# Performance work log

Hardware: AMD Instinct MI355X
Metric: run time of the kernel (lower is better)

## Reference

```python
import jax, jax.numpy as jnp
import numpy as np
from jax import lax

N_LINKS = 10000
N_PATHS = 100000
PATH_LEN = 8   # max_seq_len (all paths padded to this)
H = 32         # link/path state dim and GRU hidden size
RD = 8         # readout dim
T = 8          # message-passing rounds


def setup_inputs() -> dict:
    key = jax.random.key(0)
    ks = jax.random.split(key, 20)
    E = N_PATHS * PATH_LEN
    links = jax.random.randint(ks[0], (E,), 0, N_LINKS)
    paths = jnp.repeat(jnp.arange(N_PATHS), PATH_LEN)
    seqs = jnp.tile(jnp.arange(PATH_LEN), N_PATHS)
    link_capacity = jax.random.uniform(ks[1], (N_LINKS,), dtype=jnp.float32)
    bandwith = jax.random.uniform(ks[2], (N_PATHS,), dtype=jnp.float32)
    s = 1.0 / np.sqrt(H)
    u = lambda k, shp: jax.random.uniform(k, shp, minval=-s, maxval=s, dtype=jnp.float32)
    return {
        'links': links, 'paths': paths, 'seqs': seqs,
        'link_capacity': link_capacity, 'bandwith': bandwith,
        # path GRU (p_U) params, torch layout: [3H, in] with gate order r,z,n
        'p_Wih': u(ks[3], (3 * H, H)), 'p_Whh': u(ks[4], (3 * H, H)),
        'p_bih': u(ks[5], (3 * H,)), 'p_bhh': u(ks[6], (3 * H,)),
        # link GRU (l_U) params
        'l_Wih': u(ks[7], (3 * H, H)), 'l_Whh': u(ks[8], (3 * H, H)),
        'l_bih': u(ks[9], (3 * H,)), 'l_bhh': u(ks[10], (3 * H,)),
        # readout MLP
        'W1': u(ks[11], (RD, H)), 'b1': u(ks[12], (RD,)),
        'W2': u(ks[13], (RD, RD)), 'b2': u(ks[14], (RD,)),
        'W3': u(ks[15], (1, RD)), 'b3': u(ks[16], (1,)),
    }


def gru_cell(x, h, Wih, Whh, bih, bhh):
    # torch GRU cell: gates in order (reset, update, new)
    gi = x @ Wih.T + bih   # [N, 3H]
    gh = h @ Whh.T + bhh   # [N, 3H]
    i_r, i_z, i_n = jnp.split(gi, 3, axis=-1)
    h_r, h_z, h_n = jnp.split(gh, 3, axis=-1)
    r = jax.nn.sigmoid(i_r + h_r)
    z = jax.nn.sigmoid(i_z + h_z)
    n = jnp.tanh(i_n + r * h_n)
    return (1.0 - z) * n + z * h


def reference(links, paths, seqs, link_capacity, bandwith,
              p_Wih, p_Whh, p_bih, p_bhh,
              l_Wih, l_Whh, l_bih, l_bhh,
              W1, b1, W2, b2, W3, b3):
    dt = link_capacity.dtype
    # initial states: feature 0 is capacity / bandwidth, rest zeros
    link_state = jnp.concatenate(
        [link_capacity[:, None], jnp.zeros((N_LINKS, H - 1), dt)], axis=1)
    path_state = jnp.concatenate(
        [bandwith[:, None], jnp.zeros((N_PATHS, H - 1), dt)], axis=1)

    def path_step(h, x_t):
        h2 = gru_cell(x_t, h, p_Wih, p_Whh, p_bih, p_bhh)
        return h2, h2

    for _ in range(T):
        # gather link states onto path hops: [E, H]
        gathered = link_state[links]
        # scatter into dense padded path-RNN input [n_paths, L, H]
        rnn_in = jnp.zeros((N_PATHS, PATH_LEN, H), dt).at[paths, seqs].set(gathered)
        # path GRU over the padded sequence, initial hidden = path_state
        path_state, hs = lax.scan(path_step, path_state,
                                  jnp.swapaxes(rnn_in, 0, 1))  # hs: [L, n_paths, H]
        # per-hop messages back to links, then scatter-add per link
        link_msgs = hs[seqs, paths]                            # [E, H]
        agg = jax.ops.segment_sum(link_msgs, links, num_segments=N_LINKS)
        # link GRU single step: input = aggregated message, hidden = link_state
        link_state = gru_cell(agg, link_state, l_Wih, l_Whh, l_bih, l_bhh)

    # readout MLP on final path state
    x = jax.nn.relu(path_state @ W1.T + b1)
    x = jax.nn.relu(x @ W2.T + b2)
    return x @ W3.T + b3  # [n_paths, 1]
```

## Files before the change

### kernel.cpp

```cpp
#include <hip/hip_runtime.h>
#include <hip/hip_bf16.h>

#define NL 10000
#define NP 100000
#define PLEN 8
#define H 32
#define NROUNDS 8
#define E_TOT (NP * PLEN)

typedef float f2 __attribute__((ext_vector_type(2)));
typedef float f4 __attribute__((ext_vector_type(4)));
typedef short bh8 __attribute__((ext_vector_type(8)));

#define LINK_OFF   0
#define PATH_OFF   320000
#define AGG_OFF    3520000
#define WTS_OFF    3840000
#define PW_OFF     3853400
#define FLAG_OFF   3869000
#define INT_OFF    3870000
#define HS_OFF     4700032
#define WS_NEED_FLOATS (HS_OFF + (size_t)E_TOT * H)

#define LOG2E 1.44269504f


__device__ __forceinline__ float bf2f(unsigned short u) {
  union { unsigned int i; float f; } v; v.i = ((unsigned int)u) << 16; return v.f;
}
__device__ __forceinline__ float fast_exp2(float x) {
#if __has_builtin(__builtin_amdgcn_exp2f)
  return __builtin_amdgcn_exp2f(x);
#else
  return __expf(x * 0.69314718f);
#endif
}
__device__ __forceinline__ float fast_rcp(float x) {
#if __has_builtin(__builtin_amdgcn_rcpf)
  return __builtin_amdgcn_rcpf(x);
#else
  return 1.f / x;
#endif
}
__device__ __forceinline__ float fast_sigm(float x) {
  return fast_rcp(1.f + fast_exp2(-LOG2E * x));
}
__device__ __forceinline__ float fast_tanh2(float x) {
  return 1.f - 2.f * fast_rcp(1.f + fast_exp2((2.f * LOG2E) * x));
}
__device__ __forceinline__ float loadf(const void* p, long i, bool bf) {
  return bf ? bf2f(((const unsigned short*)p)[i]) : ((const float*)p)[i];
}

__device__ __forceinline__ void split8(f4 a, f4 b, bh8& hi, bh8& lo) {
  #pragma unroll
  for (int i = 0; i < 4; ++i) {
    unsigned ua = __float_as_uint(a[i]);
    float hfa = __uint_as_float(ua & 0xffff0000u);
    hi[i] = (short)(ua >> 16);
    lo[i] = (short)(__float_as_uint(a[i] - hfa) >> 16);
    unsigned ub = __float_as_uint(b[i]);
    float hfb = __uint_as_float(ub & 0xffff0000u);
    hi[4 + i] = (short)(ub >> 16);
    lo[4 + i] = (short)(__float_as_uint(b[i] - hfb) >> 16);
  }
}

__global__ void probe_dtype(const unsigned int* __restrict__ cap_words,
                            int* __restrict__ flag) {
  int lane = threadIdx.x;
  int c = 0;
  #pragma unroll
  for (int i = 0; i < 4; ++i) {
    unsigned int b = (cap_words[lane * 4 + i] >> 8) & 0xFF;
    if (b >= 0x30 && b < 0x40) ++c;
  }
  #pragma unroll
  for (int d = 32; d > 0; d >>= 1) c += __shfl_down(c, d);
  if (lane == 0) *flag = (c > 128) ? 1 : 0;
}

__device__ __forceinline__ void gru_cell_f2(const float* __restrict__ W,
                                            const f2 x[16], f2 h[16]) {
  const f2* Wih = (const f2*)W;
  const f2* Whh = (const f2*)(W + 3072);
  const float* bih = W + 6144;
  const float* bhh = W + 6240;
  f2 hn[16];
  #pragma unroll
  for (int jj = 0; jj < 16; ++jj) {
    #pragma unroll
    for (int s = 0; s < 2; ++s) {
      const int j = 2 * jj + s;
      f2 ar = {0.f, 0.f}, az = {0.f, 0.f}, an = {0.f, 0.f}, ah = {0.f, 0.f};
      #pragma unroll
      for (int k = 0; k < 16; ++k) {
        ar = __builtin_elementwise_fma(Wih[j * 16 + k], x[k], ar);
        ar = __builtin_elementwise_fma(Whh[j * 16 + k], h[k], ar);
        az = __builtin_elementwise_fma(Wih[(H + j) * 16 + k], x[k], az);
        az = __builtin_elementwise_fma(Whh[(H + j) * 16 + k], h[k], az);
        an = __builtin_elementwise_fma(Wih[(2 * H + j) * 16 + k], x[k], an);
        ah = __builtin_elementwise_fma(Whh[(2 * H + j) * 16 + k], h[k], ah);
      }
      float r = fast_sigm(ar.x + ar.y + bih[j] + bhh[j]);
      float z = fast_sigm(az.x + az.y + bih[H + j] + bhh[H + j]);
      float n = fast_tanh2(an.x + an.y + bih[2 * H + j] +
                           r * (ah.x + ah.y + bhh[2 * H + j]));
      float hold = (s == 0) ? h[jj].x : h[jj].y;
      float hv = n + z * (hold - n);
      if (s == 0) hn[jj].x = hv; else hn[jj].y = hv;
    }
  }
  #pragma unroll
  for (int k = 0; k < 16; ++k) h[k] = hn[k];
}

struct BfSeg { const void* src; int dstoff; int len; };
struct BfSegs { BfSeg s[14]; };
struct WPack { unsigned short* p[8]; };

__global__ void convert_weights(BfSegs segs, WPack wp, const int* __restrict__ flag,
                                float* __restrict__ dst) {
  const bool bf = (*flag != 0);
  const int si = blockIdx.x;
  const void* p = segs.s[si].src;
  const int off = segs.s[si].dstoff, len = segs.s[si].len;
  int hix = -1;
  if (si == 0) hix = 0; else if (si == 1) hix = 2;
  else if (si == 4) hix = 4; else if (si == 5) hix = 6;
  for (int i = threadIdx.x; i < len; i += blockDim.x) {
    float f = loadf(p, i, bf);
    dst[off + i] = f;
    if (hix >= 0) {
      unsigned u = __float_as_uint(f);
      float fh = __uint_as_float(u & 0xffff0000u);
      wp.p[hix][i] = (unsigned short)(u >> 16);
      wp.p[hix + 1][i] = (unsigned short)(__float_as_uint(f - fh) >> 16);
    }
  }
}

__global__ void init_states(const void* __restrict__ cap,
                            const void* __restrict__ bw,
                            const int* __restrict__ flag,
                            float* __restrict__ link_state,
                            unsigned short* __restrict__ lhi,
                            unsigned short* __restrict__ llo,
                            float* __restrict__ path_state) {
  const bool bf = (*flag != 0);
  int i = blockIdx.x * blockDim.x + threadIdx.x;
  if (i < NP * H) path_state[i] = ((i & (H - 1)) == 0) ? loadf(bw, i >> 5, bf) : 0.f;
  if (i < NL * H) {
    float v = ((i & (H - 1)) == 0) ? loadf(cap, i >> 5, bf) : 0.f;
    link_state[i] = v;
    unsigned u = __float_as_uint(v);
    float fh = __uint_as_float(u & 0xffff0000u);
    lhi[i] = (unsigned short)(u >> 16);
    llo[i] = (unsigned short)(__float_as_uint(v - fh) >> 16);
  }
}

__global__ void csr_count(const int* __restrict__ links, int* __restrict__ counts) {
  int e = blockIdx.x * blockDim.x + threadIdx.x;
  if (e < E_TOT) atomicAdd(&counts[links[e]], 1);
}

__global__ __launch_bounds__(256) void csr_scan(const int* __restrict__ counts,
                                                int* __restrict__ offsets,
                                                int* __restrict__ cursor) {
  __shared__ int part[256];
  const int t = threadIdx.x;
  const int base = t * 40;
  int s = 0;
  for (int i = 0; i < 40; ++i) {
    int idx = base + i;
    if (idx < NL) s += counts[idx];
  }
  part[t] = s;
  __syncthreads();
  for (int d = 1; d < 256; d <<= 1) {
    int v = (t >= d) ? part[t - d] : 0;
    __syncthreads();
    part[t] += v;
    __syncthreads();
  }
  int run = (t > 0) ? part[t - 1] : 0;
  for (int i = 0; i < 40; ++i) {
    int idx = base + i;
    if (idx < NL) {
      offsets[idx] = run;
      cursor[idx] = run;
      run += counts[idx];
    }
  }
  if (t == 255) offsets[NL] = run;
}

__global__ void csr_fill(const int* __restrict__ links, int* __restrict__ cursor,
                         int* __restrict__ perm) {
  int e = blockIdx.x * blockDim.x + threadIdx.x;
  if (e < E_TOT) {
    int l = links[e];
    int pos = atomicAdd(&cursor[l], 1);
    perm[e] = pos;
  }
}

template <int LAST>
__global__ __launch_bounds__(256) void path_round_mfma(
    const int* __restrict__ links, const int* __restrict__ perm,
    const unsigned short* __restrict__ lhi, const unsigned short* __restrict__ llo,
    float* __restrict__ path_state, float* __restrict__ hs,
    const float* __restrict__ W,
    const unsigned short* __restrict__ wih_hi, const unsigned short* __restrict__ wih_lo,
    const unsigned short* __restrict__ whh_hi, const unsigned short* __restrict__ whh_lo,
    const int* __restrict__ flag, void* __restrict__ out) {
  __shared__ float lds_all[4 * 16 * 36];
  const int wv = threadIdx.x >> 6;
  const int tile = blockIdx.x * 4 + wv;
  if (tile >= NP / 16) return;
  const int p0 = tile * 16;
  const int lane = threadIdx.x & 63;
  const int c = lane & 15, q = lane >> 4, m = c;
  float* lds = lds_all + wv * (16 * 36);

  bh8 wihH[6], wihL[6], whhH[6], whhL[6];
  #pragma unroll
  for (int tn = 0; tn < 6; ++tn) {
    size_t o = (size_t)(tn * 16 + c) * H + q * 8;
    wihH[tn] = *(const bh8*)(wih_hi + o);
    wihL[tn] = *(const bh8*)(wih_lo + o);
    whhH[tn] = *(const bh8*)(whh_hi + o);
    whhL[tn] = *(const bh8*)(whh_lo + o);
  }
  const float* bih = W + 6144;
  const float* bhh = W + 6240;
  float b_r[2], b_z[2], b_in[2], b_hn[2];
  #pragma unroll
  for (int u2 = 0; u2 < 2; ++u2) {
    int u = u2 * 16 + c;
    b_r[u2] = bih[u] + bhh[u];
    b_z[u2] = bih[32 + u] + bhh[32 + u];
    b_in[u2] = bih[64 + u];
    b_hn[u2] = bhh[64 + u];
  }
  float hC[2][4];
  #pragma unroll
  for (int u2 = 0; u2 < 2; ++u2)
    #pragma unroll
    for (int rg = 0; rg < 4; ++rg)
      hC[u2][rg] = path_state[(size_t)(p0 + q * 4 + rg) * H + u2 * 16 + c];
  f4 hfa = *(const f4*)(path_state + (size_t)(p0 + m) * H + q * 8);
  f4 hfb = *(const f4*)(path_state + (size_t)(p0 + m) * H + q * 8 + 4);
  bh8 hhi, hlo;
  split8(hfa, hfb, hhi, hlo);
  int lk[PLEN], pm[PLEN];
  {
    const int4* lp = (const int4*)(links + (size_t)(p0 + m) * PLEN);
    int4 a = lp[0], b = lp[1];
    lk[0] = a.x; lk[1] = a.y; lk[2] = a.z; lk[3] = a.w;
    lk[4] = b.x; lk[5] = b.y; lk[6] = b.z; lk[7] = b.w;
    if (!LAST) {
      const int4* qp = (const int4*)(perm + (size_t)(p0 + m) * PLEN);
      int4 e = qp[0], f = qp[1];
      pm[0] = e.x; pm[1] = e.y; pm[2] = e.z; pm[3] = e.w;
      pm[4] = f.x; pm[5] = f.y; pm[6] = f.z; pm[7] = f.w;
    }
  }
  bh8 xhi = *(const bh8*)(lhi + (size_t)lk[0] * H + q * 8);
  bh8 xlo = *(const bh8*)(llo + (size_t)lk[0] * H + q * 8);
  const f4 z4 = {0.f, 0.f, 0.f, 0.f};

  #pragma unroll 1
  for (int t = 0; t < PLEN; ++t) {
    bh8 xnhi, xnlo;
    if (t + 1 < PLEN) {
      xnhi = *(const bh8*)(lhi + (size_t)lk[t + 1] * H + q * 8);
      xnlo = *(const bh8*)(llo + (size_t)lk[t + 1] * H + q * 8);
    }
    f4 aR[2], aZ[2], aI[2], aHn[2];
    #pragma unroll
    for (int u2 = 0; u2 < 2; ++u2) {
      f4 a = z4;
      a = __builtin_amdgcn_mfma_f32_16x16x32_bf16(xhi, wihH[u2], a, 0, 0, 0);
      a = __builtin_amdgcn_mfma_f32_16x16x32_bf16(hhi, whhH[u2], a, 0, 0, 0);
      a = __builtin_amdgcn_mfma_f32_16x16x32_bf16(xlo, wihH[u2], a, 0, 0, 0);
      a = __builtin_amdgcn_mfma_f32_16x16x32_bf16(hlo, whhH[u2], a, 0, 0, 0);
      a = __builtin_amdgcn_mfma_f32_16x16x32_bf16(xhi, wihL[u2], a, 0, 0, 0);
      a = __builtin_amdgcn_mfma_f32_16x16x32_bf16(hhi, whhL[u2], a, 0, 0, 0);
      aR[u2] = a;
      f4 b = z4;
      b = __builtin_amdgcn_mfma_f32_16x16x32_bf16(xhi, wihH[2 + u2], b, 0, 0, 0);
      b = __builtin_amdgcn_mfma_f32_16x16x32_bf16(hhi, whhH[2 + u2], b, 0, 0, 0);
      b = __builtin_amdgcn_mfma_f32_16x16x32_bf16(xlo, wihH[2 + u2], b, 0, 0, 0);
      b = __builtin_amdgcn_mfma_f32_16x16x32_bf16(hlo, whhH[2 + u2], b, 0, 0, 0);
      b = __builtin_amdgcn_mfma_f32_16x16x32_bf16(xhi, wihL[2 + u2], b, 0, 0, 0);
      b = __builtin_amdgcn_mfma_f32_16x16x32_bf16(hhi, whhL[2 + u2], b, 0, 0, 0);
      aZ[u2] = b;
      f4 ci = z4;
      ci = __builtin_amdgcn_mfma_f32_16x16x32_bf16(xhi, wihH[4 + u2], ci, 0, 0, 0);
      ci = __builtin_amdgcn_mfma_f32_16x16x32_bf16(xlo, wihH[4 + u2], ci, 0, 0, 0);
      ci = __builtin_amdgcn_mfma_f32_16x16x32_bf16(xhi, wihL[4 + u2], ci, 0, 0, 0);
      aI[u2] = ci;
      f4 ch = z4;
      ch = __builtin_amdgcn_mfma_f32_16x16x32_bf16(hhi, whhH[4 + u2], ch, 0, 0, 0);
      ch = __builtin_amdgcn_mfma_f32_16x16x32_bf16(hlo, whhH[4 + u2], ch, 0, 0, 0);
      ch = __builtin_amdgcn_mfma_f32_16x16x32_bf16(hhi, whhL[4 + u2], ch, 0, 0, 0);
      aHn[u2] = ch;
    }
    #pragma unroll
    for (int u2 = 0; u2 < 2; ++u2)
      #pragma unroll
      for (int rg = 0; rg < 4; ++rg) {
        float rr = fast_sigm(aR[u2][rg] + b_r[u2]);
        float zz = fast_sigm(aZ[u2][rg] + b_z[u2]);
        float nn = fast_tanh2(fmaf(rr, aHn[u2][rg] + b_hn[u2], aI[u2][rg] + b_in[u2]));
        float hv = fmaf(zz, hC[u2][rg] - nn, nn);
        hC[u2][rg] = hv;
        lds[(q * 4 + rg) * 36 + u2 * 16 + c] = hv;
      }
    __builtin_amdgcn_wave_barrier();
    __builtin_amdgcn_s_waitcnt(0xC07F);
    f4 ha = *(const f4*)(lds + m * 36 + q * 8);
    f4 hb = *(const f4*)(lds + m * 36 + q * 8 + 4);
    __builtin_amdgcn_wave_barrier();
    if (!LAST) {
      float* hp = hs + (size_t)pm[t] * H + q * 8;
      *(f4*)hp = ha;
      *(f4*)(hp + 4) = hb;
    }
    if (t + 1 < PLEN) {
      split8(ha, hb, hhi, hlo);
      xhi = xnhi; xlo = xnlo;
    } else if (LAST) {
      const float* RW = W + 12672;
      float part[8];
      #pragma unroll
      for (int i = 0; i < 8; ++i) {
        const f4* w4 = (const f4*)(RW + i * 32 + q * 8);
        f4 wa = w4[0], wb = w4[1];
        part[i] = wa[0] * ha[0] + wa[1] * ha[1] + wa[2] * ha[2] + wa[3] * ha[3]
                + wb[0] * hb[0] + wb[1] * hb[1] + wb[2] * hb[2] + wb[3] * hb[3];
      }
      #pragma unroll
      for (int i = 0; i < 8; ++i) {
        part[i] += __shfl_xor(part[i], 16);
        part[i] += __shfl_xor(part[i], 32);
      }
      if (q == 0) {
        float y1[8], y2[8];
        #pragma unroll
        for (int i = 0; i < 8; ++i) y1[i] = fmaxf(part[i] + RW[256 + i], 0.f);
        #pragma unroll
        for (int i = 0; i < 8; ++i) {
          float a = RW[328 + i];
          #pragma unroll
          for (int k = 0; k < 8; ++k) a = fmaf(RW[264 + i * 8 + k], y1[k], a);
          y2[i] = fmaxf(a, 0.f);
        }
        float o = RW[344];
        #pragma unroll
        for (int k = 0; k < 8; ++k) o = fmaf(RW[336 + k], y2[k], o);
        if (*flag) ((__hip_bfloat16*)out)[p0 + m] = __float2bfloat16(o);
        else       ((float*)out)[p0 + m] = o;
      }
    } else {
      float* pp = path_state + (size_t)(p0 + m) * H + q * 8;
      *(f4*)pp = ha;
      *(f4*)(pp + 4) = hb;
    }
  }
}

__global__ __launch_bounds__(256) void agg_link_round(
    const int* __restrict__ offsets,
    const float* __restrict__ hs, float* __restrict__ link_state,
    unsigned short* __restrict__ lhi, unsigned short* __restrict__ llo,
    const float* __restrict__ W,
    const unsigned short* __restrict__ wih_hi, const unsigned short* __restrict__ wih_lo,
    const unsigned short* __restrict__ whh_hi, const unsigned short* __restrict__ whh_lo) {
  __shared__ float aggL[16 * 36];
  const int l0 = blockIdx.x * 16;
  const int wv = threadIdx.x >> 6;
  const int lane = threadIdx.x & 63;
  #pragma unroll 1
  for (int s = 0; s < 4; ++s) {
    const int li = wv * 4 + s;
    const int l = l0 + li;
    const int beg = offsets[l], end = offsets[l + 1];
    const f4* base4 = (const f4*)(hs + (size_t)beg * H);
    const int nvec = (end - beg) * (H / 4);
    f4 a0 = {0.f, 0.f, 0.f, 0.f}, a1 = {0.f, 0.f, 0.f, 0.f};
    int i = lane;
    for (; i + 64 < nvec; i += 128) {
      a0 += base4[i];
      a1 += base4[i + 64];
    }
    if (i < nvec) a0 += base4[i];
    a0 += a1;
    #pragma unroll
    for (int d = 32; d >= 8; d >>= 1) {
      #pragma unroll
      for (int k = 0; k < 4; ++k) a0[k] += __shfl_xor(a0[k], d);
    }
    if (lane < 8) *(f4*)(aggL + li * 36 + 4 * lane) = a0;
  }
  __syncthreads();
  if (threadIdx.x >= 64) return;
  const int c = lane & 15, q = lane >> 4, m = c;
  bh8 wihH[6], wihL[6], whhH[6], whhL[6];
  #pragma unroll
  for (int tn = 0; tn < 6; ++tn) {
    size_t o = (size_t)(tn * 16 + c) * H + q * 8;
    wihH[tn] = *(const bh8*)(wih_hi + o);
    wihL[tn] = *(const bh8*)(wih_lo + o);
    whhH[tn] = *(const bh8*)(whh_hi + o);
    whhL[tn] = *(const bh8*)(whh_lo + o);
  }
  const float* bih = W + 6144;
  const float* bhh = W + 6240;
  float b_r[2], b_z[2], b_in[2], b_hn[2];
  #pragma unroll
  for (int u2 = 0; u2 < 2; ++u2) {
    int u = u2 * 16 + c;
    b_r[u2] = bih[u] + bhh[u];
    b_z[u2] = bih[32 + u] + bhh[32 + u];
    b_in[u2] = bih[64 + u];
    b_hn[u2] = bhh[64 + u];
  }
  float hC[2][4];
  #pragma unroll
  for (int u2 = 0; u2 < 2; ++u2)
    #pragma unroll
    for (int rg = 0; rg < 4; ++rg)
      hC[u2][rg] = link_state[(size_t)(l0 + q * 4 + rg) * H + u2 * 16 + c];
  f4 xa = *(const f4*)(aggL + m * 36 + q * 8);
  f4 xb = *(const f4*)(aggL + m * 36 + q * 8 + 4);
  f4 hfa = *(const f4*)(link_state + (size_t)(l0 + m) * H + q * 8);
  f4 hfb = *(const f4*)(link_state + (size_t)(l0 + m) * H + q * 8 + 4);
  bh8 xhi, xlo, hhi, hlo;
  split8(xa, xb, xhi, xlo);
  split8(hfa, hfb, hhi, hlo);
  const f4 z4 = {0.f, 0.f, 0.f, 0.f};
  f4 aR[2], aZ[2], aI[2], aHn[2];
  #pragma unroll
  for (int u2 = 0; u2 < 2; ++u2) {
    f4 a = z4;
    a = __builtin_amdgcn_mfma_f32_16x16x32_bf16(xhi, wihH[u2], a, 0, 0, 0);
    a = __builtin_amdgcn_mfma_f32_16x16x32_bf16(hhi, whhH[u2], a, 0, 0, 0);
    a = __builtin_amdgcn_mfma_f32_16x16x32_bf16(xlo, wihH[u2], a, 0, 0, 0);
    a = __builtin_amdgcn_mfma_f32_16x16x32_bf16(hlo, whhH[u2], a, 0, 0, 0);
    a = __builtin_amdgcn_mfma_f32_16x16x32_bf16(xhi, wihL[u2], a, 0, 0, 0);
    a = __builtin_amdgcn_mfma_f32_16x16x32_bf16(hhi, whhL[u2], a, 0, 0, 0);
    aR[u2] = a;
    f4 b = z4;
    b = __builtin_amdgcn_mfma_f32_16x16x32_bf16(xhi, wihH[2 + u2], b, 0, 0, 0);
    b = __builtin_amdgcn_mfma_f32_16x16x32_bf16(hhi, whhH[2 + u2], b, 0, 0, 0);
    b = __builtin_amdgcn_mfma_f32_16x16x32_bf16(xlo, wihH[2 + u2], b, 0, 0, 0);
    b = __builtin_amdgcn_mfma_f32_16x16x32_bf16(hlo, whhH[2 + u2], b, 0, 0, 0);
    b = __builtin_amdgcn_mfma_f32_16x16x32_bf16(xhi, wihL[2 + u2], b, 0, 0, 0);
    b = __builtin_amdgcn_mfma_f32_16x16x32_bf16(hhi, whhL[2 + u2], b, 0, 0, 0);
    aZ[u2] = b;
    f4 ci = z4;
    ci = __builtin_amdgcn_mfma_f32_16x16x32_bf16(xhi, wihH[4 + u2], ci, 0, 0, 0);
    ci = __builtin_amdgcn_mfma_f32_16x16x32_bf16(xlo, wihH[4 + u2], ci, 0, 0, 0);
    ci = __builtin_amdgcn_mfma_f32_16x16x32_bf16(xhi, wihL[4 + u2], ci, 0, 0, 0);
    aI[u2] = ci;
    f4 ch = z4;
    ch = __builtin_amdgcn_mfma_f32_16x16x32_bf16(hhi, whhH[4 + u2], ch, 0, 0, 0);
    ch = __builtin_amdgcn_mfma_f32_16x16x32_bf16(hlo, whhH[4 + u2], ch, 0, 0, 0);
    ch = __builtin_amdgcn_mfma_f32_16x16x32_bf16(hhi, whhL[4 + u2], ch, 0, 0, 0);
    aHn[u2] = ch;
  }
  #pragma unroll
  for (int u2 = 0; u2 < 2; ++u2)
    #pragma unroll
    for (int rg = 0; rg < 4; ++rg) {
      float rr = fast_sigm(aR[u2][rg] + b_r[u2]);
      float zz = fast_sigm(aZ[u2][rg] + b_z[u2]);
      float nn = fast_tanh2(fmaf(rr, aHn[u2][rg] + b_hn[u2], aI[u2][rg] + b_in[u2]));
      float hv = fmaf(zz, hC[u2][rg] - nn, nn);
      size_t idx = (size_t)(l0 + q * 4 + rg) * H + u2 * 16 + c;
      link_state[idx] = hv;
      unsigned u = __float_as_uint(hv);
      float fh = __uint_as_float(u & 0xffff0000u);
      lhi[idx] = (unsigned short)(u >> 16);
      llo[idx] = (unsigned short)(__float_as_uint(hv - fh) >> 16);
    }
}

__global__ __launch_bounds__(64) void path_round_atomic(
    const int* __restrict__ links, const float* __restrict__ link_state,
    float* __restrict__ path_state, float* __restrict__ agg,
    const float* __restrict__ W, int do_scatter) {
  int p = blockIdx.x * 64 + threadIdx.x;
  if (p >= NP) return;
  f2 h[16];
  const f2* ps2 = (const f2*)(path_state + (size_t)p * H);
  #pragma unroll
  for (int k = 0; k < 16; ++k) h[k] = ps2[k];
  int lk[PLEN];
  const int4* lp = (const int4*)(links + (size_t)p * PLEN);
  int4 la = lp[0], lb = lp[1];
  lk[0] = la.x; lk[1] = la.y; lk[2] = la.z; lk[3] = la.w;
  lk[4] = lb.x; lk[5] = lb.y; lk[6] = lb.z; lk[7] = lb.w;
  #pragma unroll 1
  for (int t = 0; t < PLEN; ++t) {
    const f2* xs = (const f2*)(link_state + (size_t)lk[t] * H);
    f2 x[16];
    #pragma unroll
    for (int k = 0; k < 16; ++k) x[k] = xs[k];
    gru_cell_f2(W, x, h);
    if (do_scatter) {
      float* dst = agg + (size_t)lk[t] * H;
      #pragma unroll
      for (int k = 0; k < 16; ++k) {
        unsafeAtomicAdd(dst + 2 * k, h[k].x);
        unsafeAtomicAdd(dst + 2 * k + 1, h[k].y);
      }
    }
  }
  f2* po = (f2*)(path_state + (size_t)p * H);
  #pragma unroll
  for (int k = 0; k < 16; ++k) po[k] = h[k];
}

__global__ __launch_bounds__(64) void link_round_scalar(
    const float* __restrict__ agg, float* __restrict__ link_state,
    const float* __restrict__ W) {
  int li = blockIdx.x * 64 + threadIdx.x;
  if (li >= NL) return;
  f2 x[16], h[16];
  const f2* xa = (const f2*)(agg + (size_t)li * H);
  f2* hsrow = (f2*)(link_state + (size_t)li * H);
  #pragma unroll
  for (int k = 0; k < 16; ++k) { x[k] = xa[k]; h[k] = hsrow[k]; }
  gru_cell_f2(W, x, h);
  #pragma unroll
  for (int k = 0; k < 16; ++k) hsrow[k] = h[k];
}

__global__ __launch_bounds__(256) void readout_kernel(
    const float* __restrict__ path_state, const float* __restrict__ W,
    const int* __restrict__ flag, void* __restrict__ out) {
  int p = blockIdx.x * 256 + threadIdx.x;
  if (p >= NP) return;
  const float* W1 = W;
  const float* b1 = W + 256;
  const float* W2 = W + 264;
  const float* b2 = W + 328;
  const float* W3 = W + 336;
  const float* b3 = W + 344;
  float xv[32];
  const float4* xp = (const float4*)(path_state + (size_t)p * H);
  #pragma unroll
  for (int k = 0; k < 8; ++k) {
    float4 v = xp[k];
    xv[4 * k] = v.x; xv[4 * k + 1] = v.y; xv[4 * k + 2] = v.z; xv[4 * k + 3] = v.w;
  }
  float y1[8];
  #pragma unroll
  for (int i = 0; i < 8; ++i) {
    float a = b1[i];
    #pragma unroll
    for (int k = 0; k < 32; ++k) a = fmaf(W1[i * 32 + k], xv[k], a);
    y1[i] = fmaxf(a, 0.f);
  }
  float y2[8];
  #pragma unroll
  for (int i = 0; i < 8; ++i) {
    float a = b2[i];
    #pragma unroll
    for (int k = 0; k < 8; ++k) a = fmaf(W2[i * 8 + k], y1[k], a);
    y2[i] = fmaxf(a, 0.f);
  }
  float o = b3[0];
  #pragma unroll
  for (int k = 0; k < 8; ++k) o = fmaf(W3[k], y2[k], o);
  if (*flag) ((__hip_bfloat16*)out)[p] = __float2bfloat16(o);
  else       ((float*)out)[p] = o;
}

extern "C" void kernel_launch(void* const* d_in, const int* in_sizes, int n_in,
                              void* d_out, int out_size, void* d_ws, size_t ws_size,
                              hipStream_t stream) {
  (void)in_sizes; (void)n_in; (void)out_size;
  const int* links = (const int*)d_in[0];
  const void* cap = d_in[3];
  const void* bw  = d_in[4];

  float* ws = (float*)d_ws;
  float* link_state = ws + LINK_OFF;
  float* path_state = ws + PATH_OFF;
  float* agg        = ws + AGG_OFF;
  unsigned short* lhi = (unsigned short*)(ws + AGG_OFF);
  unsigned short* llo = (unsigned short*)(ws + AGG_OFF + 160000);
  float* wts        = ws + WTS_OFF;
  int*   flag       = (int*)(ws + FLAG_OFF);
  int*   ibase      = (int*)(ws + INT_OFF);
  int*   counts     = ibase;
  int*   offsets    = ibase + 10000;
  int*   cursor     = ibase + 20016;
  int*   perm       = ibase + 30016;
  float* hs         = ws + HS_OFF;

  WPack wp;
  for (int i = 0; i < 8; ++i)
    wp.p[i] = (unsigned short*)(ws + PW_OFF + i * 1600);

  const bool use_gather = ws_size >= WS_NEED_FLOATS * sizeof(float);

  probe_dtype<<<1, 64, 0, stream>>>((const unsigned int*)cap, flag);

  BfSegs segs;
  const int srcidx[14] = {5, 6, 7, 8, 9, 10, 11, 12, 13, 14, 15, 16, 17, 18};
  const int offs[14]   = {0, 3072, 6144, 6240, 6336, 9408, 12480, 12576,
                          12672, 12928, 12936, 13000, 13008, 13016};
  const int lens[14]   = {3072, 3072, 96, 96, 3072, 3072, 96, 96,
                          256, 8, 64, 8, 8, 1};
  for (int i = 0; i < 14; ++i) {
    segs.s[i].src = d_in[srcidx[i]];
    segs.s[i].dstoff = offs[i];
    segs.s[i].len = lens[i];
  }
  convert_weights<<<14, 256, 0, stream>>>(segs, wp, flag, wts);
  init_states<<<(NP * H + 255) / 256, 256, 0, stream>>>(
      cap, bw, flag, link_state, lhi, llo, path_state);

  if (use_gather) {
    hipMemsetAsync(counts, 0, NL * sizeof(int), stream);
    csr_count<<<(E_TOT + 255) / 256, 256, 0, stream>>>(links, counts);
    csr_scan<<<1, 256, 0, stream>>>(counts, offsets, cursor);
    csr_fill<<<(E_TOT + 255) / 256, 256, 0, stream>>>(links, cursor, perm);

    const int path_blocks = (NP / 16 + 3) / 4;
    for (int r = 0; r < NROUNDS - 1; ++r) {
      path_round_mfma<0><<<path_blocks, 256, 0, stream>>>(
          links, perm, lhi, llo, path_state, hs, wts,
          wp.p[0], wp.p[1], wp.p[2], wp.p[3], flag, d_out);
      agg_link_round<<<NL / 16, 256, 0, stream>>>(
          offsets, hs, link_state, lhi, llo,
          wts + 6336, wp.p[4], wp.p[5], wp.p[6], wp.p[7]);
    }
    path_round_mfma<1><<<path_blocks, 256, 0, stream>>>(
        links, perm, lhi, llo, path_state, hs, wts,
        wp.p[0], wp.p[1], wp.p[2], wp.p[3], flag, d_out);
  } else {
    for (int r = 0; r < NROUNDS; ++r) {
      const int last = (r == NROUNDS - 1);
      if (!last) hipMemsetAsync(agg, 0, NL * H * sizeof(float), stream);
      path_round_atomic<<<(NP + 63) / 64, 64, 0, stream>>>(
          links, link_state, path_state, agg, wts, !last);
      if (!last)
        link_round_scalar<<<(NL + 63) / 64, 64, 0, stream>>>(agg, link_state, wts + 6336);
    }
    readout_kernel<<<(NP + 255) / 256, 256, 0, stream>>>(
        path_state, wts + 12672, flag, d_out);
  }
}
```

Baseline: 777.7 us.

## Process two 16-path tiles per wave in path GRU kernel for ILP

New measurement: 935.0 us. 20.2% more time.

```diff
diff --git a/kernel.cpp b/kernel.cpp
--- a/kernel.cpp
+++ b/kernel.cpp
@@ -215,14 +215,13 @@
     const unsigned short* __restrict__ wih_hi, const unsigned short* __restrict__ wih_lo,
     const unsigned short* __restrict__ whh_hi, const unsigned short* __restrict__ whh_lo,
     const int* __restrict__ flag, void* __restrict__ out) {
-  __shared__ float lds_all[4 * 16 * 36];
+  __shared__ float lds_all[4 * 2 * 16 * 36];
   const int wv = threadIdx.x >> 6;
-  const int tile = blockIdx.x * 4 + wv;
-  if (tile >= NP / 16) return;
-  const int p0 = tile * 16;
+  const int pair = blockIdx.x * 4 + wv;
+  if (pair >= NP / 32) return;
   const int lane = threadIdx.x & 63;
   const int c = lane & 15, q = lane >> 4, m = c;
-  float* lds = lds_all + wv * (16 * 36);
+  float* ldsw = lds_all + wv * (2 * 16 * 36);
 
   bh8 wihH[6], wihL[6], whhH[6], whhL[6];
   #pragma unroll
@@ -244,130 +243,157 @@
     b_in[u2] = bih[64 + u];
     b_hn[u2] = bhh[64 + u];
   }
-  float hC[2][4];
-  #pragma unroll
-  for (int u2 = 0; u2 < 2; ++u2)
-    #pragma unroll
-    for (int rg = 0; rg < 4; ++rg)
-      hC[u2][rg] = path_state[(size_t)(p0 + q * 4 + rg) * H + u2 * 16 + c];
-  f4 hfa = *(const f4*)(path_state + (size_t)(p0 + m) * H + q * 8);
-  f4 hfb = *(const f4*)(path_state + (size_t)(p0 + m) * H + q * 8 + 4);
-  bh8 hhi, hlo;
-  split8(hfa, hfb, hhi, hlo);
-  int lk[PLEN], pm[PLEN];
-  {
-    const int4* lp = (const int4*)(links + (size_t)(p0 + m) * PLEN);
-    int4 a = lp[0], b = lp[1];
-    lk[0] = a.x; lk[1] = a.y; lk[2] = a.z; lk[3] = a.w;
-    lk[4] = b.x; lk[5] = b.y; lk[6] = b.z; lk[7] = b.w;
-    if (!LAST) {
-      const int4* qp = (const int4*)(perm + (size_t)(p0 + m) * PLEN);
-      int4 e = qp[0], f = qp[1];
-      pm[0] = e.x; pm[1] = e.y; pm[2] = e.z; pm[3] = e.w;
-      pm[4] = f.x; pm[5] = f.y; pm[6] = f.z; pm[7] = f.w;
-    }
-  }
-  bh8 xhi = *(const bh8*)(lhi + (size_t)lk[0] * H + q * 8);
-  bh8 xlo = *(const bh8*)(llo + (size_t)lk[0] * H + q * 8);
+
+  const int prow0 = pair * 32;
+  int pbase[2] = {prow0 + m, prow0 + 16 + m};
+
+  float hC[2][2][4];
+  bh8 hhi[2], hlo[2], xhi[2], xlo[2];
+  int iA[2];
+  #pragma unroll
+  for (int tt = 0; tt < 2; ++tt) {
+    const int prow = prow0 + tt * 16;
+    #pragma unroll
+    for (int u2 = 0; u2 < 2; ++u2)
+      #pragma unroll
+      for (int rg = 0; rg < 4; ++rg)
+        hC[tt][u2][rg] = path_state[(size_t)(prow + q * 4 + rg) * H + u2 * 16 + c];
+    f4 hfa = *(const f4*)(path_state + (size_t)(prow + m) * H + q * 8);
+    f4 hfb = *(const f4*)(path_state + (size_t)(prow + m) * H + q * 8 + 4);
+    split8(hfa, hfb, hhi[tt], hlo[tt]);
+    int i0 = links[(size_t)pbase[tt] * PLEN + 0];
+    iA[tt]  = links[(size_t)pbase[tt] * PLEN + 1];
+    xhi[tt] = *(const bh8*)(lhi + (size_t)i0 * H + q * 8);
+    xlo[tt] = *(const bh8*)(llo + (size_t)i0 * H + q * 8);
+  }
   const f4 z4 = {0.f, 0.f, 0.f, 0.f};
 
   #pragma unroll 1
   for (int t = 0; t < PLEN; ++t) {
-    bh8 xnhi, xnlo;
-    if (t + 1 < PLEN) {
-      xnhi = *(const bh8*)(lhi + (size_t)lk[t + 1] * H + q * 8);
-      xnlo = *(const bh8*)(llo + (size_t)lk[t + 1] * H + q * 8);
-    }
-    f4 aR[2], aZ[2], aI[2], aHn[2];
-    #pragma unroll
-    for (int u2 = 0; u2 < 2; ++u2) {
-      f4 a = z4;
-      a = __builtin_amdgcn_mfma_f32_16x16x32_bf16(xhi, wihH[u2], a, 0, 0, 0);
-      a = __builtin_amdgcn_mfma_f32_16x16x32_bf16(hhi, whhH[u2], a, 0, 0, 0);
-      a = __builtin_amdgcn_mfma_f32_16x16x32_bf16(xlo, wihH[u2], a, 0, 0, 0);
-      a = __builtin_amdgcn_mfma_f32_16x16x32_bf16(hlo, whhH[u2], a, 0, 0, 0);
-      a = __builtin_amdgcn_mfma_f32_16x16x32_bf16(xhi, wihL[u2], a, 0, 0, 0);
-      a = __builtin_amdgcn_mfma_f32_16x16x32_bf16(hhi, whhL[u2], a, 0, 0, 0);
-      aR[u2] = a;
-      f4 b = z4;
-      b = __builtin_amdgcn_mfma_f32_16x16x32_bf16(xhi, wihH[2 + u2], b, 0, 0, 0);
-      b = __builtin_amdgcn_mfma_f32_16x16x32_bf16(hhi, whhH[2 + u2], b, 0, 0, 0);
-      b = __builtin_amdgcn_mfma_f32_16x16x32_bf16(xlo, wihH[2 + u2], b, 0, 0, 0);
-      b = __builtin_amdgcn_mfma_f32_16x16x32_bf16(hlo, whhH[2 + u2], b, 0, 0, 0);
-      b = __builtin_amdgcn_mfma_f32_16x16x32_bf16(xhi, wihL[2 + u2], b, 0, 0, 0);
-      b = __builtin_amdgcn_mfma_f32_16x16x32_bf16(hhi, whhL[2 + u2], b, 0, 0, 0);
-      aZ[u2] = b;
-      f4 ci = z4;
-      ci = __builtin_amdgcn_mfma_f32_16x16x32_bf16(xhi, wihH[4 + u2], ci, 0, 0, 0);
-      ci = __builtin_amdgcn_mfma_f32_16x16x32_bf16(xlo, wihH[4 + u2], ci, 0, 0, 0);
-      ci = __builtin_amdgcn_mfma_f32_16x16x32_bf16(xhi, wihL[4 + u2], ci, 0, 0, 0);
-      aI[u2] = ci;
-      f4 ch = z4;
-      ch = __builtin_amdgcn_mfma_f32_16x16x32_bf16(hhi, whhH[4 + u2], ch, 0, 0, 0);
-      ch = __builtin_amdgcn_mfma_f32_16x16x32_bf16(hlo, whhH[4 + u2], ch, 0, 0, 0);
-      ch = __builtin_amdgcn_mfma_f32_16x16x32_bf16(hhi, whhL[4 + u2], ch, 0, 0, 0);
-      aHn[u2] = ch;
-    }
-    #pragma unroll
-    for (int u2 = 0; u2 < 2; ++u2)
-      #pragma unroll
-      for (int rg = 0; rg < 4; ++rg) {
-        float rr = fast_sigm(aR[u2][rg] + b_r[u2]);
-        float zz = fast_sigm(aZ[u2][rg] + b_z[u2]);
-        float nn = fast_tanh2(fmaf(rr, aHn[u2][rg] + b_hn[u2], aI[u2][rg] + b_in[u2]));
-        float hv = fmaf(zz, hC[u2][rg] - nn, nn);
-        hC[u2][rg] = hv;
-        lds[(q * 4 + rg) * 36 + u2 * 16 + c] = hv;
-      }
+    int pmt[2], iB[2];
+    bh8 xnhi[2], xnlo[2];
+    #pragma unroll
+    for (int tt = 0; tt < 2; ++tt) {
+      if (!LAST) pmt[tt] = perm[(size_t)pbase[tt] * PLEN + t];
+      iB[tt] = (t + 2 < PLEN) ? links[(size_t)pbase[tt] * PLEN + t + 2] : iA[tt];
+      if (t + 1 < PLEN) {
+        xnhi[tt] = *(const bh8*)(lhi + (size_t)iA[tt] * H + q * 8);
+        xnlo[tt] = *(const bh8*)(llo + (size_t)iA[tt] * H + q * 8);
+      }
+    }
+    f4 aR[2][2], aZ[2][2], aI[2][2], aHn[2][2];
+    #pragma unroll
+    for (int tt = 0; tt < 2; ++tt)
+      #pragma unroll
+      for (int u2 = 0; u2 < 2; ++u2) {
+        f4 a = z4;
+        a = __builtin_amdgcn_mfma_f32_16x16x32_bf16(xhi[tt], wihH[u2], a, 0, 0, 0);
+        a = __builtin_amdgcn_mfma_f32_16x16x32_bf16(hhi[tt], whhH[u2], a, 0, 0, 0);
+        a = __builtin_amdgcn_mfma_f32_16x16x32_bf16(xlo[tt], wihH[u2], a, 0, 0, 0);
+        a = __builtin_amdgcn_mfma_f32_16x16x32_bf16(hlo[tt], whhH[u2], a, 0, 0, 0);
+        a = __builtin_amdgcn_mfma_f32_16x16x32_bf16(xhi[tt], wihL[u2], a, 0, 0, 0);
+        a = __builtin_amdgcn_mfma_f32_16x16x32_bf16(hhi[tt], whhL[u2], a, 0, 0, 0);
+        aR[tt][u2] = a;
+        f4 b = z4;
+        b = __builtin_amdgcn_mfma_f32_16x16x32_bf16(xhi[tt], wihH[2 + u2], b, 0, 0, 0);
+        b = __builtin_amdgcn_mfma_f32_16x16x32_bf16(hhi[tt], whhH[2 + u2], b, 0, 0, 0);
+        b = __builtin_amdgcn_mfma_f32_16x16x32_bf16(xlo[tt], wihH[2 + u2], b, 0, 0, 0);
+        b = __builtin_amdgcn_mfma_f32_16x16x32_bf16(hlo[tt], whhH[2 + u2], b, 0, 0, 0);
+        b = __builtin_amdgcn_mfma_f32_16x16x32_bf16(xhi[tt], wihL[2 + u2], b, 0, 0, 0);
+        b = __builtin_amdgcn_mfma_f32_16x16x32_bf16(hhi[tt], whhL[2 + u2], b, 0, 0, 0);
+        aZ[tt][u2] = b;
+        f4 ci = z4;
+        ci = __builtin_amdgcn_mfma_f32_16x16x32_bf16(xhi[tt], wihH[4 + u2], ci, 0, 0, 0);
+        ci = __builtin_amdgcn_mfma_f32_16x16x32_bf16(xlo[tt], wihH[4 + u2], ci, 0, 0, 0);
+        ci = __builtin_amdgcn_mfma_f32_16x16x32_bf16(xhi[tt], wihL[4 + u2], ci, 0, 0, 0);
+        aI[tt][u2] = ci;
+        f4 ch = z4;
+        ch = __builtin_amdgcn_mfma_f32_16x16x32_bf16(hhi[tt], whhH[4 + u2], ch, 0, 0, 0);
+        ch = __builtin_amdgcn_mfma_f32_16x16x32_bf16(hlo[tt], whhH[4 + u2], ch, 0, 0, 0);
+        ch = __builtin_amdgcn_mfma_f32_16x16x32_bf16(hhi[tt], whhL[4 + u2], ch, 0, 0, 0);
+        aHn[tt][u2] = ch;
+      }
+    #pragma unroll
+    for (int tt = 0; tt < 2; ++tt)
+      #pragma unroll
+      for (int u2 = 0; u2 < 2; ++u2)
+        #pragma unroll
+        for (int rg = 0; rg < 4; ++rg) {
+          float rr = fast_sigm(aR[tt][u2][rg] + b_r[u2]);
+          float zz = fast_sigm(aZ[tt][u2][rg] + b_z[u2]);
+          float nn = fast_tanh2(fmaf(rr, aHn[tt][u2][rg] + b_hn[u2],
+                                     aI[tt][u2][rg] + b_in[u2]));
+          float hv = fmaf(zz, hC[tt][u2][rg] - nn, nn);
+          hC[tt][u2][rg] = hv;
+          ldsw[tt * 576 + (q * 4 + rg) * 36 + u2 * 16 + c] = hv;
+        }
     __builtin_amdgcn_wave_barrier();
     __builtin_amdgcn_s_waitcnt(0xC07F);
-    f4 ha = *(const f4*)(lds + m * 36 + q * 8);
-    f4 hb = *(const f4*)(lds + m * 36 + q * 8 + 4);
+    f4 ha[2], hb[2];
+    #pragma unroll
+    for (int tt = 0; tt < 2; ++tt) {
+      ha[tt] = *(const f4*)(ldsw + tt * 576 + m * 36 + q * 8);
+      hb[tt] = *(const f4*)(ldsw + tt * 576 + m * 36 + q * 8 + 4);
+    }
     __builtin_amdgcn_wave_barrier();
     if (!LAST) {
-      float* hp = hs + (size_t)pm[t] * H + q * 8;
-      *(f4*)hp = ha;
-      *(f4*)(hp + 4) = hb;
+      #pragma unroll
+      for (int tt = 0; tt < 2; ++tt) {
+        float* hp = hs + (size_t)pmt[tt] * H + q * 8;
+        *(f4*)hp = ha[tt];
+        *(f4*)(hp + 4) = hb[tt];
+      }
     }
     if (t + 1 < PLEN) {
-      split8(ha, hb, hhi, hlo);
-      xhi = xnhi; xlo = xnlo;
+      #pragma unroll
+      for (int tt = 0; tt < 2; ++tt) {
+        split8(ha[tt], hb[tt], hhi[tt], hlo[tt]);
+        xhi[tt] = xnhi[tt]; xlo[tt] = xnlo[tt];
+        iA[tt] = iB[tt];
+      }
     } else if (LAST) {
       const float* RW = W + 12672;
-      float part[8];
-      #pragma unroll
-      for (int i = 0; i < 8; ++i) {
-        const f4* w4 = (const f4*)(RW + i * 32 + q * 8);
-        f4 wa = w4[0], wb = w4[1];
-        part[i] = wa[0] * ha[0] + wa[1] * ha[1] + wa[2] * ha[2] + wa[3] * ha[3]
-                + wb[0] * hb[0] + wb[1] * hb[1] + wb[2] * hb[2] + wb[3] * hb[3];
-      }
-      #pragma unroll
-      for (int i = 0; i < 8; ++i) {
-        part[i] += __shfl_xor(part[i], 16);
-        part[i] += __shfl_xor(part[i], 32);
-      }
-      if (q == 0) {
-        float y1[8], y2[8];
-        #pragma unroll
-        for (int i = 0; i < 8; ++i) y1[i] = fmaxf(part[i] + RW[256 + i], 0.f);
+      #pragma unroll
+      for (int tt = 0; tt < 2; ++tt) {
+        float part[8];
         #pragma unroll
         for (int i = 0; i < 8; ++i) {
-          float a = RW[328 + i];
+          const f4* w4 = (const f4*)(RW + i * 32 + q * 8);
+          f4 wa = w4[0], wb = w4[1];
+          part[i] = wa[0] * ha[tt][0] + wa[1] * ha[tt][1] + wa[2] * ha[tt][2] +
+                    wa[3] * ha[tt][3] + wb[0] * hb[tt][0] + wb[1] * hb[tt][1] +
+                    wb[2] * hb[tt][2] + wb[3] * hb[tt][3];
+        }
+        #pragma unroll
+        for (int i = 0; i < 8; ++i) {
+          part[i] += __shfl_xor(part[i], 16);
+          part[i] += __shfl_xor(part[i], 32);
+        }
+        if (q == 0) {
+          float y1[8], y2[8];
           #pragma unroll
-          for (int k = 0; k < 8; ++k) a = fmaf(RW[264 + i * 8 + k], y1[k], a);
-          y2[i] = fmaxf(a, 0.f);
+          for (int i = 0; i < 8; ++i) y1[i] = fmaxf(part[i] + RW[256 + i], 0.f);
+          #pragma unroll
+          for (int i = 0; i < 8; ++i) {
+            float a = RW[328 + i];
+            #pragma unroll
+            for (int k = 0; k < 8; ++k) a = fmaf(RW[264 + i * 8 + k], y1[k], a);
+            y2[i] = fmaxf(a, 0.f);
+          }
+          float o = RW[344];
+          #pragma unroll
+          for (int k = 0; k < 8; ++k) o = fmaf(RW[336 + k], y2[k], o);
+          if (*flag) ((__hip_bfloat16*)out)[pbase[tt]] = __float2bfloat16(o);
+          else       ((float*)out)[pbase[tt]] = o;
         }
-        float o = RW[344];
-        #pragma unroll
-        for (int k = 0; k < 8; ++k) o = fmaf(RW[336 + k], y2[k], o);
-        if (*flag) ((__hip_bfloat16*)out)[p0 + m] = __float2bfloat16(o);
-        else       ((float*)out)[p0 + m] = o;
       }
     } else {
-      float* pp = path_state + (size_t)(p0 + m) * H + q * 8;
-      *(f4*)pp = ha;
-      *(f4*)(pp + 4) = hb;
+      #pragma unroll
+      for (int tt = 0; tt < 2; ++tt) {
+        float* pp = path_state + (size_t)pbase[tt] * H + q * 8;
+        *(f4*)pp = ha[tt];
+        *(f4*)(pp + 4) = hb[tt];
+      }
     }
   }
 }
@@ -633,7 +659,7 @@
     csr_scan<<<1, 256, 0, stream>>>(counts, offsets, cursor);
     csr_fill<<<(E_TOT + 255) / 256, 256, 0, stream>>>(links, cursor, perm);
 
-    const int path_blocks = (NP / 16 + 3) / 4;
+    const int path_blocks = (NP / 32 + 3) / 4;
     for (int r = 0; r < NROUNDS - 1; ++r) {
       path_round_mfma<0><<<path_blocks, 256, 0, stream>>>(
           links, perm, lhi, llo, path_state, hs, wts,
```
